# Kernel optimization log

Hardware: AMD Instinct MI355X
Metric: run time of the kernel (lower is better)

Reference implementation:

```python
import jax, jax.numpy as jnp
import numpy as np

B, S, D, H = 4, 2048, 1024, 16
DH = D // H
DFF = 4 * D
EPS = 1e-7


def _layernorm(x, scale, shift):
    # Note original quirk: (normalized + shift) * scale, biased variance, eps=1e-7
    m = jnp.mean(x, axis=-1, keepdims=True)
    v = jnp.mean((x - m) ** 2, axis=-1, keepdims=True)
    return ((x - m) / jnp.sqrt(v + EPS) + shift) * scale


def _gelu(x):
    c = jnp.sqrt(jnp.asarray(2.0 / jnp.pi, dtype=x.dtype))
    return 0.5 * x * (1.0 + jnp.tanh(c * (x + 0.044715 * x ** 3)))


def setup_inputs() -> dict:
    key = jax.random.key(0)
    ks = jax.random.split(key, 8)
    s = 0.02
    return {
        "x": jax.random.normal(ks[0], (B, S, D), jnp.float32),
        "Wq": jax.random.normal(ks[1], (D, D), jnp.float32) * s,
        "Wk": jax.random.normal(ks[2], (D, D), jnp.float32) * s,
        "Wv": jax.random.normal(ks[3], (D, D), jnp.float32) * s,
        "Wo": jax.random.normal(ks[4], (D, D), jnp.float32) * s,
        "bo": jnp.zeros((D,), jnp.float32),
        "W1": jax.random.normal(ks[5], (DFF, D), jnp.float32) * s,
        "b1": jnp.zeros((DFF,), jnp.float32),
        "W2": jax.random.normal(ks[6], (D, DFF), jnp.float32) * s,
        "b2": jnp.zeros((D,), jnp.float32),
        "ln1_scale": jnp.ones((D,), jnp.float32),
        "ln1_shift": jnp.zeros((D,), jnp.float32),
        "ln2_scale": jnp.ones((D,), jnp.float32),
        "ln2_shift": jnp.zeros((D,), jnp.float32),
    }


def reference(x, Wq, Wk, Wv, Wo, bo, W1, b1, W2, b2,
              ln1_scale, ln1_shift, ln2_scale, ln2_shift):
    b, s, d = x.shape
    h = _layernorm(x, ln1_scale, ln1_shift)
    # torch Linear: y = h @ W.T
    q = (h @ Wq.T).reshape(b, s, H, DH).transpose(0, 2, 1, 3)  # bhsd
    k = (h @ Wk.T).reshape(b, s, H, DH).transpose(0, 2, 1, 3)
    v = (h @ Wv.T).reshape(b, s, H, DH).transpose(0, 2, 1, 3)
    scores = jnp.einsum('bhqd,bhkd->bhqk', q, k) / jnp.sqrt(jnp.asarray(DH, x.dtype))
    causal = jnp.tril(jnp.ones((s, s), dtype=bool))
    scores = jnp.where(causal, scores, -jnp.inf)
    attn = jax.nn.softmax(scores, axis=-1)
    ctx = jnp.einsum('bhqk,bhkd->bhqd', attn, v)
    ctx = ctx.transpose(0, 2, 1, 3).reshape(b, s, d)
    attn_out = ctx @ Wo.T + bo
    x1 = x + attn_out  # residual (dropout is identity at eval / p effectively unused)
    h2 = _layernorm(x1, ln2_scale, ln2_shift)
    ff = _gelu(h2 @ W1.T + b1) @ W2.T + b2
    return x1 + ff
```

## Files before the change

kernel.cpp:

```cpp
#include <hip/hip_runtime.h>
#include <hip/hip_bf16.h>
#include <math.h>

typedef __bf16 bf16;
typedef __bf16 bf16x2_t __attribute__((ext_vector_type(2)));
typedef __bf16 bf16x4_t __attribute__((ext_vector_type(4)));
typedef __bf16 bf16x8_t __attribute__((ext_vector_type(8)));
typedef float  floatx4  __attribute__((ext_vector_type(4)));

#define DEVI static __device__ __forceinline__

constexpr int Bb = 4, Ss = 2048, Dd = 1024, Hh = 16, DHh = 64, DFFc = 4096;
constexpr int NTOK = Bb * Ss;
constexpr int NQKV = 3072;

DEVI void gld_lds16(const void* g, void* l) {
  __builtin_amdgcn_global_load_lds(
      (const __attribute__((address_space(1))) void*)g,
      (__attribute__((address_space(3))) void*)l, 16, 0, 0);
}

DEVI float gelu_f(float x) {
  const float c = 0.7978845608028654f;
  float t = tanhf(c * (x + 0.044715f * x * x * x));
  return 0.5f * x * (1.0f + t);
}

DEVI int xcd_lin(int lin, int nwg) {
  return (lin & 7) * (nwg >> 3) + (lin >> 3);
}

struct CastArgs {
  const float* src[6];
  bf16* dst[6];
  int n[6];
};
__global__ __launch_bounds__(256) void cast_w_kernel(CastArgs a) {
  const int which = blockIdx.y;
  const int idx = (blockIdx.x * 256 + threadIdx.x) * 4;
  if (idx >= a.n[which]) return;
  float4 v = *(const float4*)(a.src[which] + idx);
  bf16x4_t o = {(bf16)v.x, (bf16)v.y, (bf16)v.z, (bf16)v.w};
  *(bf16x4_t*)(a.dst[which] + idx) = o;
}

template <typename TIN>
__global__ __launch_bounds__(256) void ln_kernel(const TIN* __restrict__ x,
                                                 const float* __restrict__ sc,
                                                 const float* __restrict__ sh,
                                                 bf16* __restrict__ out) {
  __shared__ float rs[4], rs2[4];
  const int row = blockIdx.x, t = threadIdx.x;
  const TIN* xr = x + (size_t)row * Dd;
  float v[4];
  if constexpr (sizeof(TIN) == 2) {
    bf16x4_t tmp = *(const bf16x4_t*)((const bf16*)xr + t * 4);
#pragma unroll
    for (int i = 0; i < 4; i++) v[i] = (float)tmp[i];
  } else {
    float4 tmp = *(const float4*)((const float*)xr + t * 4);
    v[0] = tmp.x; v[1] = tmp.y; v[2] = tmp.z; v[3] = tmp.w;
  }
  float s = v[0] + v[1] + v[2] + v[3];
  float s2 = v[0] * v[0] + v[1] * v[1] + v[2] * v[2] + v[3] * v[3];
#pragma unroll
  for (int off = 1; off < 64; off <<= 1) {
    s += __shfl_xor(s, off);
    s2 += __shfl_xor(s2, off);
  }
  if ((t & 63) == 0) { rs[t >> 6] = s; rs2[t >> 6] = s2; }
  __syncthreads();
  float S1 = rs[0] + rs[1] + rs[2] + rs[3];
  float S2 = rs2[0] + rs2[1] + rs2[2] + rs2[3];
  float mean = S1 * (1.0f / Dd);
  float var = S2 * (1.0f / Dd) - mean * mean;
  float rinv = rsqrtf(var + 1e-7f);
#pragma unroll
  for (int i = 0; i < 4; i++) {
    int c = t * 4 + i;
    out[(size_t)row * Dd + c] = (bf16)(((v[i] - mean) * rinv + sh[c]) * sc[c]);
  }
}

template <int BN, int MODE>
__global__ __launch_bounds__(512, 2) void gemmk(const bf16* __restrict__ A,
                                                const bf16* __restrict__ Bw,
                                                const float* __restrict__ bias,
                                                const void* __restrict__ res,
                                                void* __restrict__ outp,
                                                int M, int N, int K) {
  constexpr int BUNITS = BN / 64;
  constexpr int AELEM = 16384;
  constexpr int BELEM = BUNITS * 4096;
  constexpr int WN = (BN == 256) ? 4 : 2;
  constexpr int WM = 8 / WN;
  constexpr int WR_H = 256 / WM;
  constexpr int M_rep = WR_H / 16;
  constexpr int NPH = M_rep / 2;
  __shared__ bf16 lds[2 * (AELEM + BELEM)];
  bf16* Ab = lds;
  bf16* Bl = lds + 2 * AELEM;

  const int tid = threadIdx.x;
  const int w = tid >> 6, lane = tid & 63;
  const int quad = lane >> 4, l16 = lane & 15;
  const int l7x8 = (lane & 7) << 3;
  const int wr = w / WN, wc = w % WN;

  const int gx = (int)gridDim.x;
  const int nwg = gx * (int)gridDim.y;
  const int lin = xcd_lin((int)blockIdx.y * gx + (int)blockIdx.x, nwg);
  const int m0 = (lin / gx) * 256;
  const int n0 = (lin % gx) * BN;

  const int s0 = w * 1024 + lane * 16;
  const int sr = s0 >> 7;
  const int sc = ((s0 ^ ((sr & 7) << 4)) & 127) >> 1;
  const int toff = w * 512 + lane * 8;

  const bf16* Agu[4];
  const bf16* Bgu[BUNITS];
#pragma unroll
  for (int u = 0; u < 4; ++u) Agu[u] = A + (size_t)(m0 + u * 64 + sr) * K + sc;
#pragma unroll
  for (int u = 0; u < BUNITS; ++u)
    Bgu[u] = Bw + (size_t)(n0 + u * 64 + sr) * K + sc;

  auto issA = [&](int t, int lo) {
    const int q = t & 1, ko = t * 64;
#pragma unroll
    for (int u = 0; u < 2; ++u)
      gld_lds16(Agu[lo + u] + ko, Ab + q * AELEM + (lo + u) * 4096 + toff);
  };
  auto issB = [&](int t, int lo, int cnt) {
    const int q = t & 1, ko = t * 64;
#pragma unroll 2
    for (int u = 0; u < cnt; ++u)
      gld_lds16(Bgu[lo + u] + ko, Bl + q * BELEM + (lo + u) * 4096 + toff);
  };

  auto rdA = [&](int q, int mi, int kk) {
    const int r = wr * WR_H + mi * 16 + l16;
    return *(const bf16x8_t*)(Ab + q * AELEM + (r >> 6) * 4096 + (r & 63) * 64 +
                              ((quad * 8 + kk * 32) ^ l7x8));
  };
  auto rdB = [&](int q, int j, int kk) {
    const int r = wc * 64 + j * 16 + l16;
    return *(const bf16x8_t*)(Bl + q * BELEM + (r >> 6) * 4096 + (r & 63) * 64 +
                              ((quad * 8 + kk * 32) ^ l7x8));
  };

  floatx4 acc[M_rep][4] = {};
  const int NT = K >> 6;

  issA(0, 0); issA(0, 2); issB(0, 0, BUNITS);
  issA(1, 0);
  if (BN == 256) {
    issB(1, 0, 2);
    asm volatile("s_waitcnt vmcnt(4)" ::: "memory");
  } else {
    asm volatile("s_waitcnt vmcnt(2)" ::: "memory");
  }
  __builtin_amdgcn_sched_barrier(0);
  __builtin_amdgcn_s_barrier();
  __builtin_amdgcn_sched_barrier(0);

  for (int t = 0; t < NT; ++t) {
    const int q = t & 1;
    bf16x8_t bfv[4][2];
#pragma unroll
    for (int p = 0; p < NPH; ++p) {
      bf16x8_t af[2][2];
#pragma unroll
      for (int im = 0; im < 2; ++im)
#pragma unroll
        for (int kk = 0; kk < 2; ++kk)
          af[im][kk] = rdA(q, p * 2 + im, kk);
      if (p == 0) {
#pragma unroll
        for (int j = 0; j < 4; ++j)
#pragma unroll
          for (int kk = 0; kk < 2; ++kk)
            bfv[j][kk] = rdB(q, j, kk);
        if (t + 1 < NT) {
          issA(t + 1, 2);
          if (BN == 256) issB(t + 1, 2, 2);
          else issB(t + 1, 0, 2);
        }
      }
      __builtin_amdgcn_s_barrier();
      __builtin_amdgcn_sched_barrier(0);
      __builtin_amdgcn_s_setprio(1);
#pragma unroll
      for (int im = 0; im < 2; ++im)
#pragma unroll
        for (int j = 0; j < 4; ++j)
#pragma unroll
          for (int kk = 0; kk < 2; ++kk)
            acc[p * 2 + im][j] = __builtin_amdgcn_mfma_f32_16x16x32_bf16(
                af[im][kk], bfv[j][kk], acc[p * 2 + im][j], 0, 0, 0);
      __builtin_amdgcn_s_setprio(0);
      if (p == NPH - 1) {
        if (t + 2 < NT) {
          issA(t + 2, 0);
          if (BN == 256) issB(t + 2, 0, 2);
          if (BN == 256) asm volatile("s_waitcnt vmcnt(4)" ::: "memory");
          else           asm volatile("s_waitcnt vmcnt(2)" ::: "memory");
        } else {
          asm volatile("s_waitcnt vmcnt(0)" ::: "memory");
        }
        __builtin_amdgcn_sched_barrier(0);
      }
      __builtin_amdgcn_s_barrier();
      __builtin_amdgcn_sched_barrier(0);
    }
  }

#pragma unroll
  for (int i = 0; i < M_rep; ++i) {
    const int rbase = m0 + wr * WR_H + i * 16 + quad * 4;
#pragma unroll
    for (int j2 = 0; j2 < 4; ++j2) {
      const int col = n0 + wc * 64 + j2 * 16 + l16;
      float bv = 0.f;
      if constexpr (MODE == 1 || MODE == 2 || MODE == 3) bv = bias[col];
#pragma unroll
      for (int r = 0; r < 4; ++r) {
        const int row = rbase + r;
        float vacc = acc[i][j2][r] + bv;
        if constexpr (MODE == 0) {
          ((bf16*)outp)[(size_t)row * N + col] = (bf16)vacc;
        } else if constexpr (MODE == 1) {
          float xres = ((const float*)res)[(size_t)row * N + col];
          ((bf16*)outp)[(size_t)row * N + col] = (bf16)(xres + vacc);
        } else if constexpr (MODE == 2) {
          ((bf16*)outp)[(size_t)row * N + col] = (bf16)gelu_f(vacc);
        } else {
          float xres = (float)((const bf16*)res)[(size_t)row * N + col];
          ((float*)outp)[(size_t)row * N + col] = xres + vacc;
        }
      }
    }
  }
}

__global__ __launch_bounds__(256) void attn_kernel(const bf16* __restrict__ QKV,
                                                   bf16* __restrict__ ctx) {
  __shared__ bf16 Ks[64 * 72];
  __shared__ bf16 Vt[64 * 72];
  __shared__ bf16 Ps[4][2][16 * 72];

  const int tid = threadIdx.x;
  const int wave = tid >> 6, lane = tid & 63;
  const int quad = lane >> 4, l16 = lane & 15;
  const int lin = xcd_lin((int)blockIdx.y * 8 + (int)blockIdx.x, 8 * Bb * Hh);
  const int gsel = lin & 7;
  const int bh = lin >> 3;
  const int bsel = bh >> 4, hsel = bh & 15;
  const size_t base = ((size_t)bsel * Ss) * NQKV + (size_t)hsel * 64;
  const bf16* Qp = QKV + base;
  const bf16* Kp = QKV + base + 1024;
  const bf16* Vp = QKV + base + 2048;

  const int kr0 = tid >> 3, kc0 = (tid & 7) * 8;
  const int vp2 = tid & 31, vs = tid >> 5;

  for (int pass = 0; pass < 2; ++pass) {
    const int g2 = (pass == 0) ? gsel : 15 - gsel;
    const int tA = 2 * g2, tB = tA + 1;
    const int q0A = tA * 64, q0B = q0A + 64;

    const int qrA = q0A + wave * 16 + l16;
    const int qrB = q0B + wave * 16 + l16;
    bf16x8_t qA0 = *(const bf16x8_t*)(Qp + (size_t)qrA * NQKV + quad * 8);
    bf16x8_t qA1 = *(const bf16x8_t*)(Qp + (size_t)qrA * NQKV + 32 + quad * 8);
    bf16x8_t qB0 = *(const bf16x8_t*)(Qp + (size_t)qrB * NQKV + quad * 8);
    bf16x8_t qB1 = *(const bf16x8_t*)(Qp + (size_t)qrB * NQKV + 32 + quad * 8);
#pragma unroll
    for (int i = 0; i < 8; i++) {
      qA0[i] = (bf16)((float)qA0[i] * 0.125f);
      qA1[i] = (bf16)((float)qA1[i] * 0.125f);
      qB0[i] = (bf16)((float)qB0[i] * 0.125f);
      qB1[i] = (bf16)((float)qB1[i] * 0.125f);
    }

    floatx4 oA[4] = {}, oB[4] = {};
    float lA[4] = {0.f, 0.f, 0.f, 0.f}, lB[4] = {0.f, 0.f, 0.f, 0.f};

    {
      bf16x8_t k0 = *(const bf16x8_t*)(Kp + (size_t)kr0 * NQKV + kc0);
      bf16x8_t k1 = *(const bf16x8_t*)(Kp + (size_t)(kr0 + 32) * NQKV + kc0);
      const bf16* v0p = Vp + (size_t)(2 * vp2) * NQKV + vs * 8;
      bf16x8_t va = *(const bf16x8_t*)(v0p);
      bf16x8_t vb = *(const bf16x8_t*)(v0p + NQKV);
      *(bf16x8_t*)(Ks + kr0 * 72 + kc0) = k0;
      *(bf16x8_t*)(Ks + (kr0 + 32) * 72 + kc0) = k1;
#pragma unroll
      for (int i = 0; i < 8; i++) {
        bf16x2_t p2 = {va[i], vb[i]};
        *(bf16x2_t*)(Vt + (vs * 8 + i) * 72 + 2 * vp2) = p2;
      }
      __syncthreads();
    }

    auto do_sm = [&](floatx4* sg, float* l_i, bf16* pw, int q0c, bool diag,
                     int kc) {
      if (diag) {
#pragma unroll
        for (int r = 0; r < 4; r++) {
          const int rq = q0c + wave * 16 + quad * 4 + r;
          float p[4];
          float rsum = 0.f;
#pragma unroll
          for (int g = 0; g < 4; g++) {
            float v = (kc + g * 16 + l16 > rq) ? -1e30f : sg[g][r];
            p[g] = __expf(v);
            rsum += p[g];
          }
          rsum += __shfl_xor(rsum, 1);
          rsum += __shfl_xor(rsum, 2);
          rsum += __shfl_xor(rsum, 4);
          rsum += __shfl_xor(rsum, 8);
          l_i[r] += rsum;
#pragma unroll
          for (int g = 0; g < 4; g++)
            pw[(quad * 4 + r) * 72 + g * 16 + l16] = (bf16)p[g];
        }
      } else {
#pragma unroll
        for (int r = 0; r < 4; r++) {
          float p[4];
          float rsum = 0.f;
#pragma unroll
          for (int g = 0; g < 4; g++) {
            p[g] = __expf(sg[g][r]);
            rsum += p[g];
          }
          rsum += __shfl_xor(rsum, 1);
          rsum += __shfl_xor(rsum, 2);
          rsum += __shfl_xor(rsum, 4);
          rsum += __shfl_xor(rsum, 8);
          l_i[r] += rsum;
#pragma unroll
          for (int g = 0; g < 4; g++)
            pw[(quad * 4 + r) * 72 + g * 16 + l16] = (bf16)p[g];
        }
      }
    };

    const int ntiles = tB + 1;
    for (int it = 0; it < ntiles; ++it) {
      const int kc = it * 64;
      const bool more = (it + 1) < ntiles;
      const bool aAct = (it <= tA);

      bf16x8_t nk0, nk1, nva, nvb;
      if (more) {
        const int kn = kc + 64;
        nk0 = *(const bf16x8_t*)(Kp + (size_t)(kn + kr0) * NQKV + kc0);
        nk1 = *(const bf16x8_t*)(Kp + (size_t)(kn + kr0 + 32) * NQKV + kc0);
        const bf16* v0p = Vp + (size_t)(kn + 2 * vp2) * NQKV + vs * 8;
        nva = *(const bf16x8_t*)(v0p);
        nvb = *(const bf16x8_t*)(v0p + NQKV);
      }

      floatx4 sA[4], sB[4];
      __builtin_amdgcn_s_setprio(1);
#pragma unroll
      for (int g = 0; g < 4; g++) {
        bf16x8_t ka = *(const bf16x8_t*)(Ks + (g * 16 + l16) * 72 + quad * 8);
        bf16x8_t kb = *(const bf16x8_t*)(Ks + (g * 16 + l16) * 72 + 32 + quad * 8);
        floatx4 z = {0.f, 0.f, 0.f, 0.f};
        if (aAct) {
          floatx4 s = __builtin_amdgcn_mfma_f32_16x16x32_bf16(qA0, ka, z, 0, 0, 0);
          sA[g] = __builtin_amdgcn_mfma_f32_16x16x32_bf16(qA1, kb, s, 0, 0, 0);
        }
        floatx4 s2 = __builtin_amdgcn_mfma_f32_16x16x32_bf16(qB0, ka, z, 0, 0, 0);
        sB[g] = __builtin_amdgcn_mfma_f32_16x16x32_bf16(qB1, kb, s2, 0, 0, 0);
      }
      __builtin_amdgcn_s_setprio(0);

      if (aAct) do_sm(sA, lA, &Ps[wave][0][0], q0A, it == tA, kc);
      do_sm(sB, lB, &Ps[wave][1][0], q0B, it == tB, kc);

      bf16x8_t pA0, pA1;
      if (aAct) {
        pA0 = *(const bf16x8_t*)(&Ps[wave][0][0] + l16 * 72 + quad * 8);
        pA1 = *(const bf16x8_t*)(&Ps[wave][0][0] + l16 * 72 + 32 + quad * 8);
      }
      bf16x8_t pB0 = *(const bf16x8_t*)(&Ps[wave][1][0] + l16 * 72 + quad * 8);
      bf16x8_t pB1 = *(const bf16x8_t*)(&Ps[wave][1][0] + l16 * 72 + 32 + quad * 8);
      __builtin_amdgcn_s_setprio(1);
#pragma unroll
      for (int nt = 0; nt < 4; nt++) {
        bf16x8_t vf0 = *(const bf16x8_t*)(Vt + (nt * 16 + l16) * 72 + quad * 8);
        bf16x8_t vf1 = *(const bf16x8_t*)(Vt + (nt * 16 + l16) * 72 + 32 + quad * 8);
        if (aAct) {
          oA[nt] = __builtin_amdgcn_mfma_f32_16x16x32_bf16(pA0, vf0, oA[nt], 0, 0, 0);
          oA[nt] = __builtin_amdgcn_mfma_f32_16x16x32_bf16(pA1, vf1, oA[nt], 0, 0, 0);
        }
        oB[nt] = __builtin_amdgcn_mfma_f32_16x16x32_bf16(pB0, vf0, oB[nt], 0, 0, 0);
        oB[nt] = __builtin_amdgcn_mfma_f32_16x16x32_bf16(pB1, vf1, oB[nt], 0, 0, 0);
      }
      __builtin_amdgcn_s_setprio(0);

      __syncthreads();
      if (more) {
        *(bf16x8_t*)(Ks + kr0 * 72 + kc0) = nk0;
        *(bf16x8_t*)(Ks + (kr0 + 32) * 72 + kc0) = nk1;
#pragma unroll
        for (int i = 0; i < 8; i++) {
          bf16x2_t p2 = {nva[i], nvb[i]};
          *(bf16x2_t*)(Vt + (vs * 8 + i) * 72 + 2 * vp2) = p2;
        }
        __syncthreads();
      }
    }

#pragma unroll
    for (int nt = 0; nt < 4; nt++)
#pragma unroll
      for (int r = 0; r < 4; r++) {
        const int rqA = q0A + wave * 16 + quad * 4 + r;
        const int rqB = q0B + wave * 16 + quad * 4 + r;
        size_t aa = ((size_t)bsel * Ss + rqA) * Dd + (size_t)hsel * DHh + nt * 16 + l16;
        size_t ab = ((size_t)bsel * Ss + rqB) * Dd + (size_t)hsel * DHh + nt * 16 + l16;
        ctx[aa] = (bf16)(oA[nt][r] / lA[r]);
        ctx[ab] = (bf16)(oB[nt][r] / lB[r]);
      }
  }
}

extern "C" void kernel_launch(void* const* d_in, const int* in_sizes, int n_in,
                              void* d_out, int out_size, void* d_ws, size_t ws_size,
                              hipStream_t stream) {
  (void)in_sizes; (void)n_in; (void)out_size; (void)ws_size;
  const float* x = (const float*)d_in[0];
  const float* Wq = (const float*)d_in[1];
  const float* Wk = (const float*)d_in[2];
  const float* Wv = (const float*)d_in[3];
  const float* Wo = (const float*)d_in[4];
  const float* bo = (const float*)d_in[5];
  const float* W1 = (const float*)d_in[6];
  const float* b1 = (const float*)d_in[7];
  const float* W2 = (const float*)d_in[8];
  const float* b2 = (const float*)d_in[9];
  const float* ln1s = (const float*)d_in[10];
  const float* ln1b = (const float*)d_in[11];
  const float* ln2s = (const float*)d_in[12];
  const float* ln2b = (const float*)d_in[13];

  char* wsb = (char*)d_ws;
  const size_t MB = 1024 * 1024;
  bf16* Wqb = (bf16*)(wsb);
  bf16* Wkb = (bf16*)(wsb + 2 * MB);
  bf16* Wvb = (bf16*)(wsb + 4 * MB);
  bf16* Wob = (bf16*)(wsb + 6 * MB);
  bf16* W1b = (bf16*)(wsb + 8 * MB);
  bf16* W2b = (bf16*)(wsb + 16 * MB);
  bf16* h   = (bf16*)(wsb + 24 * MB);
  bf16* qkv = (bf16*)(wsb + 40 * MB);
  bf16* ctx = (bf16*)(wsb + 88 * MB);
  bf16* x1  = (bf16*)(wsb + 104 * MB);
  bf16* h2  = ctx;
  bf16* ff1 = h;

  dim3 blk(256, 1, 1);
  dim3 blk8(512, 1, 1);

  CastArgs ca;
  ca.src[0] = Wq; ca.src[1] = Wk; ca.src[2] = Wv; ca.src[3] = Wo;
  ca.src[4] = W1; ca.src[5] = W2;
  ca.dst[0] = Wqb; ca.dst[1] = Wkb; ca.dst[2] = Wvb; ca.dst[3] = Wob;
  ca.dst[4] = W1b; ca.dst[5] = W2b;
  ca.n[0] = ca.n[1] = ca.n[2] = ca.n[3] = Dd * Dd;
  ca.n[4] = ca.n[5] = Dd * DFFc;
  cast_w_kernel<<<dim3((Dd * DFFc) / (256 * 4), 6, 1), blk, 0, stream>>>(ca);

  ln_kernel<float><<<dim3(NTOK, 1, 1), blk, 0, stream>>>(x, ln1s, ln1b, h);
  gemmk<256, 0><<<dim3(12, NTOK / 256, 1), blk8, 0, stream>>>(h, Wqb, nullptr, nullptr,
                                                              qkv, NTOK, NQKV, Dd);
  attn_kernel<<<dim3(8, Bb * Hh, 1), blk, 0, stream>>>(qkv, ctx);
  gemmk<128, 1><<<dim3(8, NTOK / 256, 1), blk8, 0, stream>>>(ctx, Wob, bo, x, x1,
                                                             NTOK, Dd, Dd);
  ln_kernel<bf16><<<dim3(NTOK, 1, 1), blk, 0, stream>>>(x1, ln2s, ln2b, h2);
  gemmk<256, 2><<<dim3(16, NTOK / 256, 1), blk8, 0, stream>>>(h2, W1b, b1, nullptr, ff1,
                                                              NTOK, DFFc, Dd);
  gemmk<128, 3><<<dim3(8, NTOK / 256, 1), blk8, 0, stream>>>(ff1, W2b, b2, x1,
                                                             (float*)d_out, NTOK, Dd, DFFc);
}
```

Measured before the change: 493.0 us.

## Restructure GEMM main loop with triple buffering for narrow tiles and finer phases

Rewrites the GEMM K-loop schedule. BN=128 tiles now use a three-stage LDS ring with prefetch two tiles ahead, split into two k-halves. BN=256 tiles keep double buffering but split each K tile into four MFMA phases with interleaved LDS reads and staggered global-to-LDS issues. The aim is to hide global load latency and reduce register pressure from holding both k-halves of the fragments. The cost is more LDS for the triple buffer and more barriers, and the vmcnt accounting must match exactly or correctness breaks.

```diff
diff --git a/kernel.cpp b/kernel.cpp
--- a/kernel.cpp
+++ b/kernel.cpp
@@ -89,17 +89,16 @@
                                                 const void* __restrict__ res,
                                                 void* __restrict__ outp,
                                                 int M, int N, int K) {
+  constexpr int NBUF = (BN == 256) ? 2 : 3;
   constexpr int BUNITS = BN / 64;
   constexpr int AELEM = 16384;
   constexpr int BELEM = BUNITS * 4096;
   constexpr int WN = (BN == 256) ? 4 : 2;
-  constexpr int WM = 8 / WN;
-  constexpr int WR_H = 256 / WM;
+  constexpr int WR_H = (BN == 256) ? 128 : 64;
   constexpr int M_rep = WR_H / 16;
-  constexpr int NPH = M_rep / 2;
-  __shared__ bf16 lds[2 * (AELEM + BELEM)];
+  __shared__ bf16 lds[NBUF * (AELEM + BELEM)];
   bf16* Ab = lds;
-  bf16* Bl = lds + 2 * AELEM;
+  bf16* Bl = lds + NBUF * AELEM;
 
   const int tid = threadIdx.x;
   const int w = tid >> 6, lane = tid & 63;
@@ -126,93 +125,150 @@
   for (int u = 0; u < BUNITS; ++u)
     Bgu[u] = Bw + (size_t)(n0 + u * 64 + sr) * K + sc;
 
-  auto issA = [&](int t, int lo) {
-    const int q = t & 1, ko = t * 64;
-#pragma unroll
-    for (int u = 0; u < 2; ++u)
-      gld_lds16(Agu[lo + u] + ko, Ab + q * AELEM + (lo + u) * 4096 + toff);
+  auto stA = [&](int t, int u) {
+    gld_lds16(Agu[u] + t * 64, Ab + (t % NBUF) * AELEM + u * 4096 + toff);
   };
-  auto issB = [&](int t, int lo, int cnt) {
-    const int q = t & 1, ko = t * 64;
-#pragma unroll 2
-    for (int u = 0; u < cnt; ++u)
-      gld_lds16(Bgu[lo + u] + ko, Bl + q * BELEM + (lo + u) * 4096 + toff);
+  auto stB = [&](int t, int u) {
+    gld_lds16(Bgu[u] + t * 64, Bl + (t % NBUF) * BELEM + u * 4096 + toff);
   };
-
-  auto rdA = [&](int q, int mi, int kk) {
+  auto rdA = [&](int buf, int mi, int kk) {
     const int r = wr * WR_H + mi * 16 + l16;
-    return *(const bf16x8_t*)(Ab + q * AELEM + (r >> 6) * 4096 + (r & 63) * 64 +
-                              ((quad * 8 + kk * 32) ^ l7x8));
+    return *(const bf16x8_t*)(Ab + buf * AELEM + (r >> 6) * 4096 +
+                              (r & 63) * 64 + ((quad * 8 + kk * 32) ^ l7x8));
   };
-  auto rdB = [&](int q, int j, int kk) {
+  auto rdB = [&](int buf, int j, int kk) {
     const int r = wc * 64 + j * 16 + l16;
-    return *(const bf16x8_t*)(Bl + q * BELEM + (r >> 6) * 4096 + (r & 63) * 64 +
-                              ((quad * 8 + kk * 32) ^ l7x8));
+    return *(const bf16x8_t*)(Bl + buf * BELEM + (r >> 6) * 4096 +
+                              (r & 63) * 64 + ((quad * 8 + kk * 32) ^ l7x8));
   };
 
   floatx4 acc[M_rep][4] = {};
   const int NT = K >> 6;
 
-  issA(0, 0); issA(0, 2); issB(0, 0, BUNITS);
-  issA(1, 0);
-  if (BN == 256) {
-    issB(1, 0, 2);
-    asm volatile("s_waitcnt vmcnt(4)" ::: "memory");
+  if constexpr (BN == 256) {
+#pragma unroll
+    for (int u = 0; u < 4; ++u) stA(0, u);
+#pragma unroll
+    for (int u = 0; u < 4; ++u) stB(0, u);
+    stA(1, 0); stA(1, 2);
+#pragma unroll
+    for (int u = 0; u < 4; ++u) stB(1, u);
   } else {
-    asm volatile("s_waitcnt vmcnt(2)" ::: "memory");
-  }
+#pragma unroll
+    for (int u = 0; u < 4; ++u) stA(0, u);
+    stB(0, 0); stB(0, 1);
+#pragma unroll
+    for (int u = 0; u < 4; ++u) stA(1, u);
+    stB(1, 0); stB(1, 1);
+  }
+  asm volatile("s_waitcnt vmcnt(6)" ::: "memory");
   __builtin_amdgcn_sched_barrier(0);
   __builtin_amdgcn_s_barrier();
-  __builtin_amdgcn_sched_barrier(0);
 
   for (int t = 0; t < NT; ++t) {
-    const int q = t & 1;
-    bf16x8_t bfv[4][2];
-#pragma unroll
-    for (int p = 0; p < NPH; ++p) {
-      bf16x8_t af[2][2];
-#pragma unroll
-      for (int im = 0; im < 2; ++im)
-#pragma unroll
-        for (int kk = 0; kk < 2; ++kk)
-          af[im][kk] = rdA(q, p * 2 + im, kk);
-      if (p == 0) {
+    const int buf = t % NBUF;
+    bf16x8_t a[4], b[4];
+
+    if constexpr (BN == 256) {
+#pragma unroll
+      for (int mi = 0; mi < 4; ++mi) a[mi] = rdA(buf, mi, 0);
+#pragma unroll
+      for (int j = 0; j < 4; ++j) b[j] = rdB(buf, j, 0);
+      if (t + 1 < NT) { stA(t + 1, 1); stA(t + 1, 3); }
+      __builtin_amdgcn_s_barrier();
+      __builtin_amdgcn_s_setprio(1);
+#pragma unroll
+      for (int mi = 0; mi < 4; ++mi)
 #pragma unroll
         for (int j = 0; j < 4; ++j)
-#pragma unroll
-          for (int kk = 0; kk < 2; ++kk)
-            bfv[j][kk] = rdB(q, j, kk);
-        if (t + 1 < NT) {
-          issA(t + 1, 2);
-          if (BN == 256) issB(t + 1, 2, 2);
-          else issB(t + 1, 0, 2);
-        }
-      }
-      __builtin_amdgcn_s_barrier();
+          acc[mi][j] = __builtin_amdgcn_mfma_f32_16x16x32_bf16(a[mi], b[j],
+                                                               acc[mi][j], 0, 0, 0);
+      __builtin_amdgcn_s_setprio(0);
+      __builtin_amdgcn_s_barrier();
+#pragma unroll
+      for (int mi = 0; mi < 4; ++mi) a[mi] = rdA(buf, 4 + mi, 0);
+      __builtin_amdgcn_s_barrier();
+      __builtin_amdgcn_s_setprio(1);
+#pragma unroll
+      for (int mi = 0; mi < 4; ++mi)
+#pragma unroll
+        for (int j = 0; j < 4; ++j)
+          acc[4 + mi][j] = __builtin_amdgcn_mfma_f32_16x16x32_bf16(
+              a[mi], b[j], acc[4 + mi][j], 0, 0, 0);
+      __builtin_amdgcn_s_setprio(0);
+      __builtin_amdgcn_s_barrier();
+#pragma unroll
+      for (int mi = 0; mi < 4; ++mi) a[mi] = rdA(buf, mi, 1);
+#pragma unroll
+      for (int j = 0; j < 4; ++j) b[j] = rdB(buf, j, 1);
+      __builtin_amdgcn_s_barrier();
+      __builtin_amdgcn_s_setprio(1);
+#pragma unroll
+      for (int mi = 0; mi < 4; ++mi)
+#pragma unroll
+        for (int j = 0; j < 4; ++j)
+          acc[mi][j] = __builtin_amdgcn_mfma_f32_16x16x32_bf16(a[mi], b[j],
+                                                               acc[mi][j], 0, 0, 0);
+      __builtin_amdgcn_s_setprio(0);
+      __builtin_amdgcn_s_barrier();
+#pragma unroll
+      for (int mi = 0; mi < 4; ++mi) a[mi] = rdA(buf, 4 + mi, 1);
+      __builtin_amdgcn_s_barrier();
+      __builtin_amdgcn_s_setprio(1);
+#pragma unroll
+      for (int mi = 0; mi < 4; ++mi)
+#pragma unroll
+        for (int j = 0; j < 4; ++j)
+          acc[4 + mi][j] = __builtin_amdgcn_mfma_f32_16x16x32_bf16(
+              a[mi], b[j], acc[4 + mi][j], 0, 0, 0);
+      __builtin_amdgcn_s_setprio(0);
+      if (t + 2 < NT) {
+        stA(t + 2, 0); stA(t + 2, 2);
+#pragma unroll
+        for (int u = 0; u < 4; ++u) stB(t + 2, u);
+        asm volatile("s_waitcnt vmcnt(6)" ::: "memory");
+      } else {
+        asm volatile("s_waitcnt vmcnt(0)" ::: "memory");
+      }
       __builtin_amdgcn_sched_barrier(0);
-      __builtin_amdgcn_s_setprio(1);
-#pragma unroll
-      for (int im = 0; im < 2; ++im)
+      __builtin_amdgcn_s_barrier();
+    } else {
+#pragma unroll
+      for (int mi = 0; mi < 4; ++mi) a[mi] = rdA(buf, mi, 0);
+#pragma unroll
+      for (int j = 0; j < 4; ++j) b[j] = rdB(buf, j, 0);
+      if (t + 2 < NT) { stA(t + 2, 0); stA(t + 2, 1); stB(t + 2, 0); }
+      __builtin_amdgcn_s_barrier();
+      __builtin_amdgcn_s_setprio(1);
+#pragma unroll
+      for (int mi = 0; mi < 4; ++mi)
 #pragma unroll
         for (int j = 0; j < 4; ++j)
-#pragma unroll
-          for (int kk = 0; kk < 2; ++kk)
-            acc[p * 2 + im][j] = __builtin_amdgcn_mfma_f32_16x16x32_bf16(
-                af[im][kk], bfv[j][kk], acc[p * 2 + im][j], 0, 0, 0);
-      __builtin_amdgcn_s_setprio(0);
-      if (p == NPH - 1) {
-        if (t + 2 < NT) {
-          issA(t + 2, 0);
-          if (BN == 256) issB(t + 2, 0, 2);
-          if (BN == 256) asm volatile("s_waitcnt vmcnt(4)" ::: "memory");
-          else           asm volatile("s_waitcnt vmcnt(2)" ::: "memory");
-        } else {
-          asm volatile("s_waitcnt vmcnt(0)" ::: "memory");
-        }
-        __builtin_amdgcn_sched_barrier(0);
-      }
-      __builtin_amdgcn_s_barrier();
+          acc[mi][j] = __builtin_amdgcn_mfma_f32_16x16x32_bf16(a[mi], b[j],
+                                                               acc[mi][j], 0, 0, 0);
+      __builtin_amdgcn_s_setprio(0);
+      __builtin_amdgcn_s_barrier();
+#pragma unroll
+      for (int mi = 0; mi < 4; ++mi) a[mi] = rdA(buf, mi, 1);
+#pragma unroll
+      for (int j = 0; j < 4; ++j) b[j] = rdB(buf, j, 1);
+      if (t + 2 < NT) { stA(t + 2, 2); stA(t + 2, 3); stB(t + 2, 1); }
+      __builtin_amdgcn_s_barrier();
+      __builtin_amdgcn_s_setprio(1);
+#pragma unroll
+      for (int mi = 0; mi < 4; ++mi)
+#pragma unroll
+        for (int j = 0; j < 4; ++j)
+          acc[mi][j] = __builtin_amdgcn_mfma_f32_16x16x32_bf16(a[mi], b[j],
+                                                               acc[mi][j], 0, 0, 0);
+      __builtin_amdgcn_s_setprio(0);
+      if (t + 2 < NT) {
+        asm volatile("s_waitcnt vmcnt(6)" ::: "memory");
+      } else {
+        asm volatile("s_waitcnt vmcnt(0)" ::: "memory");
+      }
       __builtin_amdgcn_sched_barrier(0);
+      __builtin_amdgcn_s_barrier();
     }
   }
 
```

Result: slower. 505.2 us (+2.5%).

## Replace 256-row GEMM tiles with 128x128 tiles and triple-buffered K=32 pipeline

Applied to the files above, without the earlier changes.

Rewrites the GEMM kernel to use 128x128 output tiles with 256-thread blocks and a three-stage LDS ring buffer over K-steps of 32. The old version used 256xBN tiles, 512 threads, a double buffer over K=64, and split-phase barriers with priority hints. The change aims to create more workgroups and raise occupancy (launch bounds 3 per CU) while keeping loads two stages ahead. In exchange each tile reuses less data, so global traffic per FLOP goes up, and the setprio and phased scheduling are dropped.

```diff
diff --git a/kernel.cpp b/kernel.cpp
--- a/kernel.cpp
+++ b/kernel.cpp
@@ -82,143 +82,95 @@
   }
 }
 
-template <int BN, int MODE>
-__global__ __launch_bounds__(512, 2) void gemmk(const bf16* __restrict__ A,
+template <int MODE>
+__global__ __launch_bounds__(256, 3) void gemmk(const bf16* __restrict__ A,
                                                 const bf16* __restrict__ Bw,
                                                 const float* __restrict__ bias,
                                                 const void* __restrict__ res,
                                                 void* __restrict__ outp,
                                                 int M, int N, int K) {
-  constexpr int BUNITS = BN / 64;
-  constexpr int AELEM = 16384;
-  constexpr int BELEM = BUNITS * 4096;
-  constexpr int WN = (BN == 256) ? 4 : 2;
-  constexpr int WM = 8 / WN;
-  constexpr int WR_H = 256 / WM;
-  constexpr int M_rep = WR_H / 16;
-  constexpr int NPH = M_rep / 2;
-  __shared__ bf16 lds[2 * (AELEM + BELEM)];
+  constexpr int TEL = 4096;
+  __shared__ bf16 lds[6 * TEL];
   bf16* Ab = lds;
-  bf16* Bl = lds + 2 * AELEM;
+  bf16* Bl = lds + 3 * TEL;
 
   const int tid = threadIdx.x;
   const int w = tid >> 6, lane = tid & 63;
   const int quad = lane >> 4, l16 = lane & 15;
-  const int l7x8 = (lane & 7) << 3;
-  const int wr = w / WN, wc = w % WN;
+  const int wr = w >> 1, wc = w & 1;
 
   const int gx = (int)gridDim.x;
   const int nwg = gx * (int)gridDim.y;
   const int lin = xcd_lin((int)blockIdx.y * gx + (int)blockIdx.x, nwg);
-  const int m0 = (lin / gx) * 256;
-  const int n0 = (lin % gx) * BN;
-
-  const int s0 = w * 1024 + lane * 16;
-  const int sr = s0 >> 7;
-  const int sc = ((s0 ^ ((sr & 7) << 4)) & 127) >> 1;
-  const int toff = w * 512 + lane * 8;
-
-  const bf16* Agu[4];
-  const bf16* Bgu[BUNITS];
-#pragma unroll
-  for (int u = 0; u < 4; ++u) Agu[u] = A + (size_t)(m0 + u * 64 + sr) * K + sc;
-#pragma unroll
-  for (int u = 0; u < BUNITS; ++u)
-    Bgu[u] = Bw + (size_t)(n0 + u * 64 + sr) * K + sc;
-
-  auto issA = [&](int t, int lo) {
-    const int q = t & 1, ko = t * 64;
-#pragma unroll
-    for (int u = 0; u < 2; ++u)
-      gld_lds16(Agu[lo + u] + ko, Ab + q * AELEM + (lo + u) * 4096 + toff);
+  const int m0 = (lin / gx) * 128;
+  const int n0 = (lin % gx) * 128;
+
+  const bf16* Aps[2];
+  const bf16* Bps[2];
+#pragma unroll
+  for (int p = 0; p < 2; ++p) {
+    const int sp = p * 4096 + tid * 16;
+    const int sr = sp >> 6;
+    const int sc = ((sp ^ (((sr >> 1) & 3) << 4)) & 63) >> 1;
+    Aps[p] = A + (size_t)(m0 + sr) * K + sc;
+    Bps[p] = Bw + (size_t)(n0 + sr) * K + sc;
+  }
+  const int dst0 = w * 512 + lane * 8;
+
+  auto stage = [&](int t) {
+    const int q = t % 3, ko = t * 32;
+#pragma unroll
+    for (int p = 0; p < 2; ++p) {
+      gld_lds16(Aps[p] + ko, Ab + q * TEL + p * 2048 + dst0);
+      gld_lds16(Bps[p] + ko, Bl + q * TEL + p * 2048 + dst0);
+    }
   };
-  auto issB = [&](int t, int lo, int cnt) {
-    const int q = t & 1, ko = t * 64;
-#pragma unroll 2
-    for (int u = 0; u < cnt; ++u)
-      gld_lds16(Bgu[lo + u] + ko, Bl + q * BELEM + (lo + u) * 4096 + toff);
+  auto rdA = [&](int q, int mi) {
+    const int r = wr * 64 + mi * 16 + l16;
+    return *(const bf16x8_t*)(Ab + q * TEL + r * 32 +
+                              ((quad * 8) ^ (((r >> 1) & 3) << 3)));
   };
-
-  auto rdA = [&](int q, int mi, int kk) {
-    const int r = wr * WR_H + mi * 16 + l16;
-    return *(const bf16x8_t*)(Ab + q * AELEM + (r >> 6) * 4096 + (r & 63) * 64 +
-                              ((quad * 8 + kk * 32) ^ l7x8));
+  auto rdB = [&](int q, int j) {
+    const int r = wc * 64 + j * 16 + l16;
+    return *(const bf16x8_t*)(Bl + q * TEL + r * 32 +
+                              ((quad * 8) ^ (((r >> 1) & 3) << 3)));
   };
-  auto rdB = [&](int q, int j, int kk) {
-    const int r = wc * 64 + j * 16 + l16;
-    return *(const bf16x8_t*)(Bl + q * BELEM + (r >> 6) * 4096 + (r & 63) * 64 +
-                              ((quad * 8 + kk * 32) ^ l7x8));
-  };
-
-  floatx4 acc[M_rep][4] = {};
-  const int NT = K >> 6;
-
-  issA(0, 0); issA(0, 2); issB(0, 0, BUNITS);
-  issA(1, 0);
-  if (BN == 256) {
-    issB(1, 0, 2);
-    asm volatile("s_waitcnt vmcnt(4)" ::: "memory");
-  } else {
-    asm volatile("s_waitcnt vmcnt(2)" ::: "memory");
-  }
+
+  floatx4 acc[4][4] = {};
+  const int NT = K >> 5;
+
+  stage(0);
+  stage(1);
+  asm volatile("s_waitcnt vmcnt(4)" ::: "memory");
   __builtin_amdgcn_sched_barrier(0);
   __builtin_amdgcn_s_barrier();
-  __builtin_amdgcn_sched_barrier(0);
 
   for (int t = 0; t < NT; ++t) {
-    const int q = t & 1;
-    bf16x8_t bfv[4][2];
-#pragma unroll
-    for (int p = 0; p < NPH; ++p) {
-      bf16x8_t af[2][2];
-#pragma unroll
-      for (int im = 0; im < 2; ++im)
-#pragma unroll
-        for (int kk = 0; kk < 2; ++kk)
-          af[im][kk] = rdA(q, p * 2 + im, kk);
-      if (p == 0) {
-#pragma unroll
-        for (int j = 0; j < 4; ++j)
-#pragma unroll
-          for (int kk = 0; kk < 2; ++kk)
-            bfv[j][kk] = rdB(q, j, kk);
-        if (t + 1 < NT) {
-          issA(t + 1, 2);
-          if (BN == 256) issB(t + 1, 2, 2);
-          else issB(t + 1, 0, 2);
-        }
-      }
-      __builtin_amdgcn_s_barrier();
-      __builtin_amdgcn_sched_barrier(0);
-      __builtin_amdgcn_s_setprio(1);
-#pragma unroll
-      for (int im = 0; im < 2; ++im)
-#pragma unroll
-        for (int j = 0; j < 4; ++j)
-#pragma unroll
-          for (int kk = 0; kk < 2; ++kk)
-            acc[p * 2 + im][j] = __builtin_amdgcn_mfma_f32_16x16x32_bf16(
-                af[im][kk], bfv[j][kk], acc[p * 2 + im][j], 0, 0, 0);
-      __builtin_amdgcn_s_setprio(0);
-      if (p == NPH - 1) {
-        if (t + 2 < NT) {
-          issA(t + 2, 0);
-          if (BN == 256) issB(t + 2, 0, 2);
-          if (BN == 256) asm volatile("s_waitcnt vmcnt(4)" ::: "memory");
-          else           asm volatile("s_waitcnt vmcnt(2)" ::: "memory");
-        } else {
-          asm volatile("s_waitcnt vmcnt(0)" ::: "memory");
-        }
-        __builtin_amdgcn_sched_barrier(0);
-      }
-      __builtin_amdgcn_s_barrier();
-      __builtin_amdgcn_sched_barrier(0);
-    }
-  }
-
-#pragma unroll
-  for (int i = 0; i < M_rep; ++i) {
-    const int rbase = m0 + wr * WR_H + i * 16 + quad * 4;
+    const int q = t % 3;
+    bf16x8_t a[4], b[4];
+#pragma unroll
+    for (int mi = 0; mi < 4; ++mi) a[mi] = rdA(q, mi);
+#pragma unroll
+    for (int j = 0; j < 4; ++j) b[j] = rdB(q, j);
+    if (t + 2 < NT) stage(t + 2);
+#pragma unroll
+    for (int mi = 0; mi < 4; ++mi)
+#pragma unroll
+      for (int j = 0; j < 4; ++j)
+        acc[mi][j] = __builtin_amdgcn_mfma_f32_16x16x32_bf16(a[mi], b[j],
+                                                             acc[mi][j], 0, 0, 0);
+    if (t + 2 < NT) {
+      asm volatile("s_waitcnt vmcnt(4)" ::: "memory");
+    } else {
+      asm volatile("s_waitcnt vmcnt(0)" ::: "memory");
+    }
+    __builtin_amdgcn_sched_barrier(0);
+    __builtin_amdgcn_s_barrier();
+  }
+
+#pragma unroll
+  for (int i = 0; i < 4; ++i) {
+    const int rbase = m0 + wr * 64 + i * 16 + quad * 4;
 #pragma unroll
     for (int j2 = 0; j2 < 4; ++j2) {
       const int col = n0 + wc * 64 + j2 * 16 + l16;
@@ -466,7 +418,6 @@
   bf16* ff1 = h;
 
   dim3 blk(256, 1, 1);
-  dim3 blk8(512, 1, 1);
 
   CastArgs ca;
   ca.src[0] = Wq; ca.src[1] = Wk; ca.src[2] = Wv; ca.src[3] = Wo;
@@ -478,14 +429,14 @@
   cast_w_kernel<<<dim3((Dd * DFFc) / (256 * 4), 6, 1), blk, 0, stream>>>(ca);
 
   ln_kernel<float><<<dim3(NTOK, 1, 1), blk, 0, stream>>>(x, ln1s, ln1b, h);
-  gemmk<256, 0><<<dim3(12, NTOK / 256, 1), blk8, 0, stream>>>(h, Wqb, nullptr, nullptr,
-                                                              qkv, NTOK, NQKV, Dd);
+  gemmk<0><<<dim3(24, NTOK / 128, 1), blk, 0, stream>>>(h, Wqb, nullptr, nullptr,
+                                                        qkv, NTOK, NQKV, Dd);
   attn_kernel<<<dim3(8, Bb * Hh, 1), blk, 0, stream>>>(qkv, ctx);
-  gemmk<128, 1><<<dim3(8, NTOK / 256, 1), blk8, 0, stream>>>(ctx, Wob, bo, x, x1,
-                                                             NTOK, Dd, Dd);
+  gemmk<1><<<dim3(8, NTOK / 128, 1), blk, 0, stream>>>(ctx, Wob, bo, x, x1,
+                                                       NTOK, Dd, Dd);
   ln_kernel<bf16><<<dim3(NTOK, 1, 1), blk, 0, stream>>>(x1, ln2s, ln2b, h2);
-  gemmk<256, 2><<<dim3(16, NTOK / 256, 1), blk8, 0, stream>>>(h2, W1b, b1, nullptr, ff1,
-                                                              NTOK, DFFc, Dd);
-  gemmk<128, 3><<<dim3(8, NTOK / 256, 1), blk8, 0, stream>>>(ff1, W2b, b2, x1,
-                                                             (float*)d_out, NTOK, Dd, DFFc);
-}
+  gemmk<2><<<dim3(32, NTOK / 128, 1), blk, 0, stream>>>(h2, W1b, b1, nullptr, ff1,
+                                                        NTOK, DFFc, Dd);
+  gemmk<3><<<dim3(8, NTOK / 128, 1), blk, 0, stream>>>(ff1, W2b, b2, x1,
+                                                       (float*)d_out, NTOK, Dd, DFFc);
+}
```

Result: slower. 513.1 us (+4.1%).
